# Kernel optimization log

Hardware: AMD Instinct MI355X
Metric: run time of the kernel (lower is better)

## Reference

```python
import jax, jax.numpy as jnp
import numpy as np

WIN_SIZE = 16

def setup_inputs() -> dict:
    key = jax.random.key(0)
    k1, k2 = jax.random.split(key)
    B, C, W, H, Wd = 8, 32, WIN_SIZE, 128, 128
    out = jax.random.normal(k1, (B, C, W, H, Wd), dtype=jnp.float32)
    target = jax.random.normal(k2, (B, C, W, H, Wd), dtype=jnp.float32)
    return {"out": out, "target": target}

def reference(out, target):
    # Even window indices j compare out[:, :, j] vs target[:, :, j+1].
    o = out[:, :, 0:WIN_SIZE:2]      # [B, C, W/2, H, Wd]
    t = target[:, :, 1:WIN_SIZE:2]   # [B, C, W/2, H, Wd]
    # MSELoss averages over (C, H, Wd) per (batch, window-slice).
    per_slice = jnp.mean((o - t) ** 2, axis=(1, 3, 4))  # [B, W/2]
    half_win = WIN_SIZE / 2.0
    loss = jnp.sum(jnp.sum(per_slice, axis=1) / half_win)
    return loss
```

## Files before the change

kernel.cpp:

```cpp
#include <hip/hip_runtime.h>


#define N4_TOTAL (2048u * 4096u)
#define INV_NORM (1.0f / 4194304.0f)

__global__ __launch_bounds__(256) void cont_loss_kernel(
    const float* __restrict__ out_p,
    const float* __restrict__ tgt_p,
    float* __restrict__ result)
{
    const float4* __restrict__ o4 = (const float4*)out_p;
    const float4* __restrict__ t4 = (const float4*)tgt_p;

    float acc = 0.0f;
    const unsigned stride = gridDim.x * blockDim.x;
    for (unsigned g = blockIdx.x * blockDim.x + threadIdx.x; g < N4_TOTAL; g += stride) {
        unsigned pair = g >> 12;
        unsigned i4   = g & 4095u;
        float4 o = o4[pair * 8192u + i4];
        float4 t = t4[pair * 8192u + 4096u + i4];
        float dx = o.x - t.x;
        float dy = o.y - t.y;
        float dz = o.z - t.z;
        float dw = o.w - t.w;
        acc = fmaf(dx, dx, acc);
        acc = fmaf(dy, dy, acc);
        acc = fmaf(dz, dz, acc);
        acc = fmaf(dw, dw, acc);
    }

    #pragma unroll
    for (int off = 32; off > 0; off >>= 1)
        acc += __shfl_down(acc, off, 64);

    __shared__ float wave_sums[4];
    const int lane = threadIdx.x & 63;
    const int wid  = threadIdx.x >> 6;
    if (lane == 0) wave_sums[wid] = acc;
    __syncthreads();

    if (threadIdx.x == 0) {
        float s = wave_sums[0] + wave_sums[1] + wave_sums[2] + wave_sums[3];
        atomicAdd(result, s * INV_NORM);
    }
}

extern "C" void kernel_launch(void* const* d_in, const int* in_sizes, int n_in,
                              void* d_out, int out_size, void* d_ws, size_t ws_size,
                              hipStream_t stream)
{
    const float* out_p = (const float*)d_in[0];
    const float* tgt_p = (const float*)d_in[1];
    float* result = (float*)d_out;

    hipMemsetAsync(result, 0, sizeof(float), stream);

    cont_loss_kernel<<<2048, 256, 0, stream>>>(out_p, tgt_p, result);
}
```

Baseline: 458.9 us.

## Unroll streaming loads with independent accumulators and use two-stage deterministic reduction

Replaces the grid-stride loop with a fully unrolled fixed sweep that issues four independent float4 load pairs per iteration into separate accumulators, increasing memory-level parallelism. The global atomicAdd and the memset are replaced by per-block partials in workspace, followed by a single-block second kernel. This removes contention on one address at the cost of an extra kernel launch and a dependency on workspace size.

```diff
diff --git a/kernel.cpp b/kernel.cpp
--- a/kernel.cpp
+++ b/kernel.cpp
@@ -1,48 +1,86 @@
 #include <hip/hip_runtime.h>
 
 
-#define N4_TOTAL (2048u * 4096u)
-#define INV_NORM (1.0f / 4194304.0f)
+#define NBLOCKS   2048u
+#define NTHREADS  256u
+#define NSWEEPS   16u
+#define SWEEP4    1048576u
+#define INV_NORM  (1.0f / 4194304.0f)
 
-__global__ __launch_bounds__(256) void cont_loss_kernel(
+__global__ __launch_bounds__(256) void cont_loss_stage1(
     const float* __restrict__ out_p,
     const float* __restrict__ tgt_p,
-    float* __restrict__ result)
+    float* __restrict__ partials)
 {
     const float4* __restrict__ o4 = (const float4*)out_p;
     const float4* __restrict__ t4 = (const float4*)tgt_p;
 
-    float acc = 0.0f;
-    const unsigned stride = gridDim.x * blockDim.x;
-    for (unsigned g = blockIdx.x * blockDim.x + threadIdx.x; g < N4_TOTAL; g += stride) {
-        unsigned pair = g >> 12;
-        unsigned i4   = g & 4095u;
-        float4 o = o4[pair * 8192u + i4];
-        float4 t = t4[pair * 8192u + 4096u + i4];
-        float dx = o.x - t.x;
-        float dy = o.y - t.y;
-        float dz = o.z - t.z;
-        float dw = o.w - t.w;
-        acc = fmaf(dx, dx, acc);
-        acc = fmaf(dy, dy, acc);
-        acc = fmaf(dz, dz, acc);
-        acc = fmaf(dw, dw, acc);
+    const unsigned g0   = blockIdx.x * NTHREADS + threadIdx.x;
+    const unsigned base = (g0 >> 12) * 8192u + (g0 & 4095u);
+
+    float acc[4] = {0.0f, 0.0f, 0.0f, 0.0f};
+
+    #pragma unroll
+    for (unsigned k = 0; k < NSWEEPS; k += 4) {
+        float4 o_[4], t_[4];
+        #pragma unroll
+        for (int j = 0; j < 4; ++j) {
+            const unsigned off = base + (k + j) * SWEEP4;
+            o_[j] = o4[off];
+            t_[j] = t4[off + 4096u];
+        }
+        #pragma unroll
+        for (int j = 0; j < 4; ++j) {
+            const float dx = o_[j].x - t_[j].x;
+            const float dy = o_[j].y - t_[j].y;
+            const float dz = o_[j].z - t_[j].z;
+            const float dw = o_[j].w - t_[j].w;
+            acc[j] = fmaf(dx, dx, acc[j]);
+            acc[j] = fmaf(dy, dy, acc[j]);
+            acc[j] = fmaf(dz, dz, acc[j]);
+            acc[j] = fmaf(dw, dw, acc[j]);
+        }
     }
+
+    float s = (acc[0] + acc[1]) + (acc[2] + acc[3]);
 
     #pragma unroll
     for (int off = 32; off > 0; off >>= 1)
-        acc += __shfl_down(acc, off, 64);
+        s += __shfl_down(s, off, 64);
 
     __shared__ float wave_sums[4];
     const int lane = threadIdx.x & 63;
     const int wid  = threadIdx.x >> 6;
-    if (lane == 0) wave_sums[wid] = acc;
+    if (lane == 0) wave_sums[wid] = s;
     __syncthreads();
 
-    if (threadIdx.x == 0) {
-        float s = wave_sums[0] + wave_sums[1] + wave_sums[2] + wave_sums[3];
-        atomicAdd(result, s * INV_NORM);
-    }
+    if (threadIdx.x == 0)
+        partials[blockIdx.x] = (wave_sums[0] + wave_sums[1]) +
+                               (wave_sums[2] + wave_sums[3]);
+}
+
+__global__ __launch_bounds__(256) void cont_loss_stage2(
+    const float* __restrict__ partials,
+    float* __restrict__ result)
+{
+    float s = 0.0f;
+    #pragma unroll
+    for (int j = 0; j < 8; ++j)
+        s += partials[threadIdx.x + j * 256];
+
+    #pragma unroll
+    for (int off = 32; off > 0; off >>= 1)
+        s += __shfl_down(s, off, 64);
+
+    __shared__ float wave_sums[4];
+    const int lane = threadIdx.x & 63;
+    const int wid  = threadIdx.x >> 6;
+    if (lane == 0) wave_sums[wid] = s;
+    __syncthreads();
+
+    if (threadIdx.x == 0)
+        result[0] = ((wave_sums[0] + wave_sums[1]) +
+                     (wave_sums[2] + wave_sums[3])) * INV_NORM;
 }
 
 extern "C" void kernel_launch(void* const* d_in, const int* in_sizes, int n_in,
@@ -51,9 +89,9 @@
 {
     const float* out_p = (const float*)d_in[0];
     const float* tgt_p = (const float*)d_in[1];
-    float* result = (float*)d_out;
+    float* result   = (float*)d_out;
+    float* partials = (float*)d_ws;
 
-    hipMemsetAsync(result, 0, sizeof(float), stream);
-
-    cont_loss_kernel<<<2048, 256, 0, stream>>>(out_p, tgt_p, result);
+    cont_loss_stage1<<<NBLOCKS, NTHREADS, 0, stream>>>(out_p, tgt_p, partials);
+    cont_loss_stage2<<<1, NTHREADS, 0, stream>>>(partials, result);
 }
```

Result: no change. 454.5 us (-1.0%).
